# Optimization experiments

Hardware: AMD Instinct MI355X
Metric: run time of the kernel (lower is better)

The kernel has to match this reference:

```python
import jax, jax.numpy as jnp
import numpy as np

B, T, F, H, O = 256, 512, 128, 256, 1


def setup_inputs() -> dict:
    key = jax.random.key(0)
    ks = jax.random.split(key, 32)
    def rn(i, shape, s=0.05):
        return jax.random.normal(ks[i], shape, jnp.float32) * s
    inp = {
        "x": jax.random.normal(ks[0], (B, T, F), jnp.float32),
        # BatchNorm1d (eval mode) params / running stats
        "bn_gamma": 1.0 + rn(1, (F,), 0.1),
        "bn_beta": rn(2, (F,), 0.1),
        "bn_mean": rn(3, (F,), 0.1),
        "bn_var": 1.0 + jax.random.uniform(ks[4], (F,), jnp.float32) * 0.5,
        # SpatialAttention linear F->F
        "sa_W": rn(5, (F, F)), "sa_b": rn(6, (F,)),
        # layer_in F->H
        "in_W": rn(7, (H, F)), "in_b": rn(8, (H,)),
        # LSTM layer 0 (input H) and layer 1 (input H), torch gate order i,f,g,o
        "Wih0": rn(9, (4 * H, H)), "Whh0": rn(10, (4 * H, H)),
        "bih0": rn(11, (4 * H,)), "bhh0": rn(12, (4 * H,)),
        "Wih1": rn(13, (4 * H, H)), "Whh1": rn(14, (4 * H, H)),
        "bih1": rn(15, (4 * H,)), "bhh1": rn(16, (4 * H,)),
        # TemporalAttention: hidden_to_input H->F, T_A F->F
        "ta_hW": rn(17, (F, H)), "ta_hb": rn(18, (F,)),
        "ta_W": rn(19, (F, F)), "ta_b": rn(20, (F,)),
        # layer_out F->O, no bias
        "out_W": rn(21, (O, F)),
    }
    return inp


def _lstm_layer(seq, Wih, Whh, bih, bhh):
    # seq: [T, B, H_in]
    Hd = Whh.shape[1]
    b = bih + bhh
    def step(carry, xt):
        h, c = carry
        g = xt @ Wih.T + h @ Whh.T + b  # [B, 4H]
        i, f, gg, o = jnp.split(g, 4, axis=-1)
        c = jax.nn.sigmoid(f) * c + jax.nn.sigmoid(i) * jnp.tanh(gg)
        h = jax.nn.sigmoid(o) * jnp.tanh(c)
        return (h, c), h
    nb = seq.shape[1]
    init = (jnp.zeros((nb, Hd), seq.dtype), jnp.zeros((nb, Hd), seq.dtype))
    _, hs = jax.lax.scan(step, init, seq)
    return hs  # [T, B, H]


def reference(x, bn_gamma, bn_beta, bn_mean, bn_var, sa_W, sa_b, in_W, in_b,
              Wih0, Whh0, bih0, bhh0, Wih1, Whh1, bih1, bhh1,
              ta_hW, ta_hb, ta_W, ta_b, out_W):
    # BatchNorm1d (eval): normalize per feature
    xb = (x - bn_mean) * jax.lax.rsqrt(bn_var + 1e-5) * bn_gamma + bn_beta
    # Spatial attention (vectorized over all timesteps at once)
    alpha = jax.nn.softmax(jax.nn.sigmoid(xb @ sa_W.T + sa_b), axis=-1)
    xs = xb * alpha
    # layer_in (dropout is identity in eval mode)
    h = xs @ in_W.T + in_b  # [B, T, H]
    seq = jnp.swapaxes(h, 0, 1)  # [T, B, H]
    seq = _lstm_layer(seq, Wih0, Whh0, bih0, bhh0)
    seq = _lstm_layer(seq, Wih1, Whh1, bih1, bhh1)
    h_t = jnp.swapaxes(seq, 0, 1)  # [B, T, H]
    # Temporal attention
    total = h_t @ ta_hW.T + ta_hb  # [B, T, F]
    beta = jax.nn.softmax(jax.nn.relu(total @ ta_W.T + ta_b), axis=1)
    ctx = jnp.sum(beta * total, axis=1)  # [B, F]
    out = (ctx @ out_W.T).squeeze()  # [B]
    return out
```

## Files before the change

kernel.cpp:

```cpp
#include <hip/hip_runtime.h>

typedef __attribute__((ext_vector_type(8))) short short8;
typedef __attribute__((ext_vector_type(4))) float floatx4;
typedef __attribute__((ext_vector_type(2))) unsigned long long ull2;

__device__ __forceinline__ unsigned short f2bf(float f) {
  unsigned int u = __float_as_uint(f);
  unsigned int lsb = (u >> 16) & 1u;
  u += 0x7fffu + lsb;
  return (unsigned short)(u >> 16);
}
__device__ __forceinline__ float bf2f(unsigned short u) {
  unsigned int x = ((unsigned int)u) << 16;
  return __uint_as_float(x);
}
__device__ __forceinline__ float sigm(float x) { return 1.f / (1.f + __expf(-x)); }
__device__ __forceinline__ float tanh_fast(float x) { return 2.f / (1.f + __expf(-2.f * x)) - 1.f; }
__device__ __forceinline__ floatx4 mfma16(short8 a, short8 b, floatx4 c) {
  return __builtin_amdgcn_mfma_f32_16x16x32_bf16(a, b, c, 0, 0, 0);
}

__global__ __launch_bounds__(256) void prep_kernel(
    const float* __restrict__ Wih0, const float* __restrict__ inW,
    const float* __restrict__ inb, const float* __restrict__ bih0,
    const float* __restrict__ bhh0, const float* __restrict__ Whh0,
    const float* __restrict__ Whh1, const float* __restrict__ Wih1,
    const float* __restrict__ tahW, const float* __restrict__ taW,
    const float* __restrict__ bih1, const float* __restrict__ bhh1,
    unsigned short* __restrict__ Wc, float* __restrict__ bc,
    unsigned short* __restrict__ Whh0b, unsigned short* __restrict__ Whh1b,
    unsigned short* __restrict__ Wih1b, unsigned short* __restrict__ tahWb,
    unsigned short* __restrict__ taWb, float* __restrict__ b1) {
  const int b = blockIdx.x, tid = threadIdx.x;
  if (b < 512) {
    const int n = b * 2 + (tid >> 7), k = tid & 127;
    float a = 0.f;
    for (int j = 0; j < 256; ++j) a += Wih0[n * 256 + j] * inW[j * 128 + k];
    Wc[n * 128 + k] = f2bf(a);
    if (k == 0) {
      float bs = bih0[n] + bhh0[n];
      for (int j = 0; j < 256; ++j) bs += Wih0[n * 256 + j] * inb[j];
      bc[n] = bs;
    }
  } else if (b < 896) {
    const int bb = b - 512;
    const float* src = (bb < 128) ? Whh0 : (bb < 256) ? Whh1 : Wih1;
    unsigned short* dst = (bb < 128) ? Whh0b : (bb < 256) ? Whh1b : Wih1b;
    const int off = (bb & 127) * 2048 + tid * 8;
    short8 v;
#pragma unroll
    for (int u = 0; u < 8; ++u) v[u] = (short)f2bf(src[off + u]);
    *(short8*)&dst[off] = v;
  } else if (b < 912) {
    const int off = (b - 896) * 2048 + tid * 8;
    short8 v;
#pragma unroll
    for (int u = 0; u < 8; ++u) v[u] = (short)f2bf(tahW[off + u]);
    *(short8*)&tahWb[off] = v;
  } else if (b < 920) {
    const int off = (b - 912) * 2048 + tid * 8;
    short8 v;
#pragma unroll
    for (int u = 0; u < 8; ++u) v[u] = (short)f2bf(taW[off + u]);
    *(short8*)&taWb[off] = v;
  } else {
#pragma unroll
    for (int u = 0; u < 4; ++u) {
      const int i = tid * 4 + u;
      b1[i] = bih1[i] + bhh1[i];
    }
  }
}

__global__ __launch_bounds__(256) void bnsa_kernel(
    const float* __restrict__ x, const float* __restrict__ gamma,
    const float* __restrict__ beta, const float* __restrict__ mean,
    const float* __restrict__ var, const float* __restrict__ saW,
    const float* __restrict__ sab, unsigned short* __restrict__ xs) {
  __shared__ unsigned short saWs[128 * 132];
  __shared__ unsigned short xbb[128 * 136];
  const int tid = threadIdx.x;
  const int wv = tid >> 6, lane = tid & 63;
  const int lm = lane & 15, q = lane >> 4;
  const long r0 = (long)blockIdx.x * 128;

  for (int i = tid; i < 16384; i += 256) saWs[(i >> 7) * 132 + (i & 127)] = f2bf(saW[i]);
  {
    const int k0 = tid & 127;
    const float mn = mean[k0];
    const float is = rsqrtf(var[k0] + 1e-5f) * gamma[k0];
    const float bt = beta[k0];
    for (int i = tid; i < 16384; i += 256) {
      const int m = i >> 7;
      xbb[m * 136 + k0] = f2bf((x[(r0 + m) * 128 + k0] - mn) * is + bt);
    }
  }
  __syncthreads();

  short8 af[2][4];
#pragma unroll
  for (int mt = 0; mt < 2; ++mt)
#pragma unroll
    for (int kt = 0; kt < 4; ++kt)
      af[mt][kt] = *(const short8*)&xbb[(wv * 32 + mt * 16 + lm) * 136 + kt * 32 + q * 8];

  floatx4 acc[2][8];
#pragma unroll
  for (int nt = 0; nt < 8; ++nt) {
    const float sb = sab[nt * 16 + lm];
    short8 bf[4];
#pragma unroll
    for (int kt = 0; kt < 4; ++kt)
      bf[kt] = *(const short8*)&saWs[(nt * 16 + lm) * 132 + kt * 32 + q * 8];
#pragma unroll
    for (int mt = 0; mt < 2; ++mt) {
      floatx4 a = (floatx4){sb, sb, sb, sb};
#pragma unroll
      for (int kt = 0; kt < 4; ++kt) a = mfma16(af[mt][kt], bf[kt], a);
      acc[mt][nt] = a;
    }
  }
  float tot[2][4];
#pragma unroll
  for (int mt = 0; mt < 2; ++mt)
#pragma unroll
    for (int r = 0; r < 4; ++r) {
      float p = 0.f;
#pragma unroll
      for (int nt = 0; nt < 8; ++nt) {
        const float e = __expf(sigm(acc[mt][nt][r]));
        acc[mt][nt][r] = e;
        p += e;
      }
      p += __shfl_xor(p, 1);
      p += __shfl_xor(p, 2);
      p += __shfl_xor(p, 4);
      p += __shfl_xor(p, 8);
      tot[mt][r] = p;
    }
  __syncthreads();
  unsigned short* stg = saWs;
#pragma unroll
  for (int nt = 0; nt < 8; ++nt) {
    const int col = nt * 16 + lm;
    const float mn = mean[col];
    const float is = rsqrtf(var[col] + 1e-5f) * gamma[col];
    const float bt = beta[col];
#pragma unroll
    for (int mt = 0; mt < 2; ++mt)
#pragma unroll
      for (int r = 0; r < 4; ++r) {
        const int row = wv * 32 + mt * 16 + q * 4 + r;
        const float xb = (x[(r0 + row) * 128 + col] - mn) * is + bt;
        stg[row * 128 + col] = f2bf(xb * (acc[mt][nt][r] / tot[mt][r]));
      }
  }
  __syncthreads();
  for (int i = tid * 8; i < 16384; i += 2048)
    *(short8*)&xs[r0 * 128 + i] = *(const short8*)&stg[i];
}

__global__ __launch_bounds__(512, 2) void persist_kernel(
    const unsigned short* __restrict__ xs,
    const unsigned short* __restrict__ Wc, const float* __restrict__ bc,
    const unsigned short* __restrict__ Whh0,
    const unsigned short* __restrict__ Wih1, const float* __restrict__ b1,
    const unsigned short* __restrict__ Whh1,
    const unsigned short* __restrict__ tahWg, const float* __restrict__ tahb,
    const unsigned short* __restrict__ taWg, const float* __restrict__ tab,
    const float* __restrict__ outW,
    ull2* __restrict__ ex,
    float* __restrict__ out) {
  __shared__ unsigned short tahWs[128 * 264];
  __shared__ unsigned short taWs[128 * 136];
  __shared__ unsigned short h0buf[16 * 264];
  __shared__ unsigned short h1buf[16 * 264];
  __shared__ float gatebuf[2][8 * 16 * 20];
  __shared__ unsigned short totB[16 * 136];

  const int tid = threadIdx.x;
  const int wv = tid >> 6, lane = tid & 63;
  const int lm = lane & 15, q = lane >> 4;
  const int slice = blockIdx.x >> 4, group = blockIdx.x & 15;
  const int g = wv & 3, ht = wv >> 2;
  const int b0 = group * 16;
  const int hcol = slice * 32 + ht * 16 + lm;
  const int ng = g * 256 + hcol;
  const int fcol = wv * 16 + lm;

  for (int i = tid; i < 128 * 256; i += 512) tahWs[(i >> 8) * 264 + (i & 255)] = tahWg[i];
  for (int i = tid; i < 128 * 128; i += 512) taWs[(i >> 7) * 136 + (i & 127)] = taWg[i];
  for (int i = tid; i < 16 * 264; i += 512) { h0buf[i] = 0; h1buf[i] = 0; }

  short8 Wcf[4], W0f[8], W1if[8], W1hf[8];
#pragma unroll
  for (int kt = 0; kt < 4; ++kt) Wcf[kt] = *(const short8*)&Wc[(size_t)ng * 128 + kt * 32 + q * 8];
#pragma unroll
  for (int kt = 0; kt < 8; ++kt) {
    W0f[kt] = *(const short8*)&Whh0[(size_t)ng * 256 + kt * 32 + q * 8];
    W1if[kt] = *(const short8*)&Wih1[(size_t)ng * 256 + kt * 32 + q * 8];
    W1hf[kt] = *(const short8*)&Whh1[(size_t)ng * 256 + kt * 32 + q * 8];
  }
  const float bcv = bc[ng], b1v = b1[ng];
  const float tahbv = tahb[fcol], tabv = tab[fcol], outWv = outW[fcol];

  floatx4 cst0 = (floatx4){0.f, 0.f, 0.f, 0.f};
  floatx4 cst1 = (floatx4){0.f, 0.f, 0.f, 0.f};
  float num[4] = {0.f, 0.f, 0.f, 0.f}, den[4] = {0.f, 0.f, 0.f, 0.f};

  const unsigned short* xrow = xs + (size_t)(b0 + lm) * 65536 + q * 8;
  short8 axf[4], axn[4];
#pragma unroll
  for (int kt = 0; kt < 4; ++kt) axf[kt] = *(const short8*)(xrow + kt * 32);

  const int ew = ((slice >> 1) << 8) + (((slice & 1) * 32 + ht * 16 + lm) << 2) + q;
  ull2* const exg = ex + (size_t)group * 2048;

  const int npidx = ((wv >> 2) << 1) | (wv & 1);
  const int nt = npidx * 64 + lane;
  unsigned voBase[8];
#pragma unroll
  for (int L = 0; L < 2; ++L)
#pragma unroll
    for (int j = 0; j < 4; ++j) voBase[L * 4 + j] = (unsigned)((L * 1024 + j * 256 + nt) << 4);
  const int cb = nt >> 2, qq = nt & 3;

  __syncthreads();

  for (int t = 0; t <= 512; ++t) {
    const int p = t & 1;
    const unsigned fvu = (unsigned)(t + 1);

    {
      floatx4 aW = (floatx4){0.f, 0.f, 0.f, 0.f};
      floatx4 aH = (floatx4){bcv, bcv, bcv, bcv};
#pragma unroll
      for (int kt = 0; kt < 4; ++kt) aW = mfma16(axf[kt], Wcf[kt], aW);
#pragma unroll
      for (int kt = 0; kt < 8; ++kt) {
        const short8 a = *(const short8*)&h0buf[lm * 264 + kt * 32 + q * 8];
        aH = mfma16(a, W0f[kt], aH);
      }
      const floatx4 acc = aW + aH;
#pragma unroll
      for (int r = 0; r < 4; ++r) gatebuf[0][(wv * 16 + q * 4 + r) * 20 + lm] = acc[r];
    }
    {
      const size_t tn = (t < 511) ? t + 1 : 511;
#pragma unroll
      for (int kt = 0; kt < 4; ++kt) axn[kt] = *(const short8*)(xrow + tn * 128 + kt * 32);
    }
    {
      floatx4 aI = (floatx4){b1v, b1v, b1v, b1v};
      floatx4 aH = (floatx4){0.f, 0.f, 0.f, 0.f};
#pragma unroll
      for (int kt = 0; kt < 8; ++kt) {
        const short8 a = *(const short8*)&h0buf[lm * 264 + kt * 32 + q * 8];
        aI = mfma16(a, W1if[kt], aI);
      }
#pragma unroll
      for (int kt = 0; kt < 8; ++kt) {
        const short8 a = *(const short8*)&h1buf[lm * 264 + kt * 32 + q * 8];
        aH = mfma16(a, W1hf[kt], aH);
      }
      const floatx4 acc = aI + aH;
#pragma unroll
      for (int r = 0; r < 4; ++r) gatebuf[1][(wv * 16 + q * 4 + r) * 20 + lm] = acc[r];
    }
    __syncthreads();

    if (g < 2) {
      const int L = g;
      unsigned short hb[4];
      if (L == 0) {
#pragma unroll
        for (int r = 0; r < 4; ++r) {
          const int m = q * 4 + r;
          const float iv = gatebuf[0][((ht * 4 + 0) * 16 + m) * 20 + lm];
          const float fv = gatebuf[0][((ht * 4 + 1) * 16 + m) * 20 + lm];
          const float gv = gatebuf[0][((ht * 4 + 2) * 16 + m) * 20 + lm];
          const float ov = gatebuf[0][((ht * 4 + 3) * 16 + m) * 20 + lm];
          const float cn = sigm(fv) * cst0[r] + sigm(iv) * tanh_fast(gv);
          cst0[r] = cn;
          hb[r] = f2bf(sigm(ov) * tanh_fast(cn));
        }
      } else {
#pragma unroll
        for (int r = 0; r < 4; ++r) hb[r] = 0;
        if (t > 0) {
#pragma unroll
          for (int r = 0; r < 4; ++r) {
            const int m = q * 4 + r;
            const float iv = gatebuf[1][((ht * 4 + 0) * 16 + m) * 20 + lm];
            const float fv = gatebuf[1][((ht * 4 + 1) * 16 + m) * 20 + lm];
            const float gv = gatebuf[1][((ht * 4 + 2) * 16 + m) * 20 + lm];
            const float ov = gatebuf[1][((ht * 4 + 3) * 16 + m) * 20 + lm];
            const float cn = sigm(fv) * cst1[r] + sigm(iv) * tanh_fast(gv);
            cst1[r] = cn;
            hb[r] = f2bf(sigm(ov) * tanh_fast(cn));
          }
        }
      }
      const unsigned long long sq = (unsigned long long)fvu << 32;
      const unsigned long long qlo = (unsigned long long)hb[0] | ((unsigned long long)hb[1] << 16) | sq;
      const unsigned long long qhi = (unsigned long long)hb[2] | ((unsigned long long)hb[3] << 16) | sq;
      unsigned long long* wp =
          (unsigned long long*)(exg + (size_t)p * 32768 + (size_t)L * 1024 + ew);
      __hip_atomic_store(&wp[0], qlo, __ATOMIC_RELAXED, __HIP_MEMORY_SCOPE_AGENT);
      __hip_atomic_store(&wp[1], qhi, __ATOMIC_RELAXED, __HIP_MEMORY_SCOPE_AGENT);
    }

    floatx4 ta;
    if (t >= 2) {
      ta = (floatx4){tahbv, tahbv, tahbv, tahbv};
#pragma unroll
      for (int kt = 0; kt < 8; ++kt) {
        const short8 a = *(const short8*)&h1buf[lm * 264 + kt * 32 + q * 8];
        ta = mfma16(a, *(const short8*)&tahWs[fcol * 264 + kt * 32 + q * 8], ta);
      }
#pragma unroll
      for (int r = 0; r < 4; ++r) totB[(q * 4 + r) * 136 + fcol] = f2bf(ta[r]);
    }
    __syncthreads();
    if (t >= 2) {
      floatx4 sa = (floatx4){tabv, tabv, tabv, tabv};
#pragma unroll
      for (int kt = 0; kt < 4; ++kt) {
        const short8 a = *(const short8*)&totB[lm * 136 + kt * 32 + q * 8];
        sa = mfma16(a, *(const short8*)&taWs[fcol * 136 + kt * 32 + q * 8], sa);
      }
#pragma unroll
      for (int r = 0; r < 4; ++r) {
        const float e = __expf(fmaxf(sa[r], 0.f));
        num[r] += e * ta[r];
        den[r] += e;
      }
    }

    if (g >= 2) {
      const unsigned pterm = (unsigned)p << 19;
      const unsigned v0o = voBase[0] + pterm, v1o = voBase[1] + pterm;
      const unsigned v2o = voBase[2] + pterm, v3o = voBase[3] + pterm;
      const unsigned v4o = voBase[4] + pterm, v5o = voBase[5] + pterm;
      const unsigned v6o = voBase[6] + pterm, v7o = voBase[7] + pterm;
      ull2 d0, d1, d2, d3, e0, e1, e2, e3;
      unsigned bad;
      do {
        asm volatile(
            "global_load_dwordx4 %0, %8, %16 sc0 sc1\n\t"
            "global_load_dwordx4 %1, %9, %16 sc0 sc1\n\t"
            "global_load_dwordx4 %2, %10, %16 sc0 sc1\n\t"
            "global_load_dwordx4 %3, %11, %16 sc0 sc1\n\t"
            "global_load_dwordx4 %4, %12, %16 sc0 sc1\n\t"
            "global_load_dwordx4 %5, %13, %16 sc0 sc1\n\t"
            "global_load_dwordx4 %6, %14, %16 sc0 sc1\n\t"
            "global_load_dwordx4 %7, %15, %16 sc0 sc1\n\t"
            "s_waitcnt vmcnt(0)"
            : "=&v"(d0), "=&v"(d1), "=&v"(d2), "=&v"(d3),
              "=&v"(e0), "=&v"(e1), "=&v"(e2), "=&v"(e3)
            : "v"(v0o), "v"(v1o), "v"(v2o), "v"(v3o),
              "v"(v4o), "v"(v5o), "v"(v6o), "v"(v7o),
              "s"(exg)
            : "memory");
        bad = ((unsigned)(d0.x >> 32) != fvu) | ((unsigned)(d0.y >> 32) != fvu) |
              ((unsigned)(d1.x >> 32) != fvu) | ((unsigned)(d1.y >> 32) != fvu) |
              ((unsigned)(d2.x >> 32) != fvu) | ((unsigned)(d2.y >> 32) != fvu) |
              ((unsigned)(d3.x >> 32) != fvu) | ((unsigned)(d3.y >> 32) != fvu) |
              ((unsigned)(e0.x >> 32) != fvu) | ((unsigned)(e0.y >> 32) != fvu) |
              ((unsigned)(e1.x >> 32) != fvu) | ((unsigned)(e1.y >> 32) != fvu) |
              ((unsigned)(e2.x >> 32) != fvu) | ((unsigned)(e2.y >> 32) != fvu) |
              ((unsigned)(e3.x >> 32) != fvu) | ((unsigned)(e3.y >> 32) != fvu);
      } while (bad);
      {
        const int c0 = cb, c1 = 64 + cb, c2 = 128 + cb, c3 = 192 + cb;
        h0buf[(qq * 4 + 0) * 264 + c0] = (unsigned short)d0.x;
        h0buf[(qq * 4 + 1) * 264 + c0] = (unsigned short)(d0.x >> 16);
        h0buf[(qq * 4 + 2) * 264 + c0] = (unsigned short)d0.y;
        h0buf[(qq * 4 + 3) * 264 + c0] = (unsigned short)(d0.y >> 16);
        h0buf[(qq * 4 + 0) * 264 + c1] = (unsigned short)d1.x;
        h0buf[(qq * 4 + 1) * 264 + c1] = (unsigned short)(d1.x >> 16);
        h0buf[(qq * 4 + 2) * 264 + c1] = (unsigned short)d1.y;
        h0buf[(qq * 4 + 3) * 264 + c1] = (unsigned short)(d1.y >> 16);
        h0buf[(qq * 4 + 0) * 264 + c2] = (unsigned short)d2.x;
        h0buf[(qq * 4 + 1) * 264 + c2] = (unsigned short)(d2.x >> 16);
        h0buf[(qq * 4 + 2) * 264 + c2] = (unsigned short)d2.y;
        h0buf[(qq * 4 + 3) * 264 + c2] = (unsigned short)(d2.y >> 16);
        h0buf[(qq * 4 + 0) * 264 + c3] = (unsigned short)d3.x;
        h0buf[(qq * 4 + 1) * 264 + c3] = (unsigned short)(d3.x >> 16);
        h0buf[(qq * 4 + 2) * 264 + c3] = (unsigned short)d3.y;
        h0buf[(qq * 4 + 3) * 264 + c3] = (unsigned short)(d3.y >> 16);
        h1buf[(qq * 4 + 0) * 264 + c0] = (unsigned short)e0.x;
        h1buf[(qq * 4 + 1) * 264 + c0] = (unsigned short)(e0.x >> 16);
        h1buf[(qq * 4 + 2) * 264 + c0] = (unsigned short)e0.y;
        h1buf[(qq * 4 + 3) * 264 + c0] = (unsigned short)(e0.y >> 16);
        h1buf[(qq * 4 + 0) * 264 + c1] = (unsigned short)e1.x;
        h1buf[(qq * 4 + 1) * 264 + c1] = (unsigned short)(e1.x >> 16);
        h1buf[(qq * 4 + 2) * 264 + c1] = (unsigned short)e1.y;
        h1buf[(qq * 4 + 3) * 264 + c1] = (unsigned short)(e1.y >> 16);
        h1buf[(qq * 4 + 0) * 264 + c2] = (unsigned short)e2.x;
        h1buf[(qq * 4 + 1) * 264 + c2] = (unsigned short)(e2.x >> 16);
        h1buf[(qq * 4 + 2) * 264 + c2] = (unsigned short)e2.y;
        h1buf[(qq * 4 + 3) * 264 + c2] = (unsigned short)(e2.y >> 16);
        h1buf[(qq * 4 + 0) * 264 + c3] = (unsigned short)e3.x;
        h1buf[(qq * 4 + 1) * 264 + c3] = (unsigned short)(e3.x >> 16);
        h1buf[(qq * 4 + 2) * 264 + c3] = (unsigned short)e3.y;
        h1buf[(qq * 4 + 3) * 264 + c3] = (unsigned short)(e3.y >> 16);
      }
    }
    __syncthreads();

#pragma unroll
    for (int kt = 0; kt < 4; ++kt) axf[kt] = axn[kt];
  }

  {
    floatx4 ta = (floatx4){tahbv, tahbv, tahbv, tahbv};
#pragma unroll
    for (int kt = 0; kt < 8; ++kt) {
      const short8 a = *(const short8*)&h1buf[lm * 264 + kt * 32 + q * 8];
      ta = mfma16(a, *(const short8*)&tahWs[fcol * 264 + kt * 32 + q * 8], ta);
    }
#pragma unroll
    for (int r = 0; r < 4; ++r) totB[(q * 4 + r) * 136 + fcol] = f2bf(ta[r]);
    __syncthreads();
    floatx4 sa = (floatx4){tabv, tabv, tabv, tabv};
#pragma unroll
    for (int kt = 0; kt < 4; ++kt) {
      const short8 a = *(const short8*)&totB[lm * 136 + kt * 32 + q * 8];
      sa = mfma16(a, *(const short8*)&taWs[fcol * 136 + kt * 32 + q * 8], sa);
    }
#pragma unroll
    for (int r = 0; r < 4; ++r) {
      const float e = __expf(fmaxf(sa[r], 0.f));
      num[r] += e * ta[r];
      den[r] += e;
    }
  }
  __syncthreads();

  float* red = &gatebuf[0][0];
#pragma unroll
  for (int r = 0; r < 4; ++r) red[(q * 4 + r) * 136 + fcol] = (num[r] / den[r]) * outWv;
  __syncthreads();
  if (slice == 0 && tid < 16) {
    float s = 0.f;
    for (int k = 0; k < 128; ++k) s += red[tid * 136 + k];
    out[b0 + tid] = s;
  }
}

extern "C" void kernel_launch(void* const* d_in, const int* in_sizes, int n_in,
                              void* d_out, int out_size, void* d_ws, size_t ws_size,
                              hipStream_t stream) {
  (void)in_sizes; (void)n_in; (void)out_size; (void)ws_size;
  const float* x    = (const float*)d_in[0];
  const float* bng  = (const float*)d_in[1];
  const float* bnb  = (const float*)d_in[2];
  const float* bnm  = (const float*)d_in[3];
  const float* bnv  = (const float*)d_in[4];
  const float* saW  = (const float*)d_in[5];
  const float* sab  = (const float*)d_in[6];
  const float* inW  = (const float*)d_in[7];
  const float* inb  = (const float*)d_in[8];
  const float* Wih0 = (const float*)d_in[9];
  const float* Whh0 = (const float*)d_in[10];
  const float* bih0 = (const float*)d_in[11];
  const float* bhh0 = (const float*)d_in[12];
  const float* Wih1 = (const float*)d_in[13];
  const float* Whh1 = (const float*)d_in[14];
  const float* bih1 = (const float*)d_in[15];
  const float* bhh1 = (const float*)d_in[16];
  const float* tahW = (const float*)d_in[17];
  const float* tahb = (const float*)d_in[18];
  const float* taW  = (const float*)d_in[19];
  const float* tab  = (const float*)d_in[20];
  const float* outW = (const float*)d_in[21];
  float* out = (float*)d_out;

  char* ws = (char*)d_ws;
  size_t off = 0;
  auto alloc = [&](size_t bytes) {
    char* p = ws + off;
    off += (bytes + 255) & ~(size_t)255;
    return p;
  };
  unsigned short* Wc    = (unsigned short*)alloc((size_t)1024 * 128 * 2);
  float* bc             = (float*)alloc(1024 * 4);
  float* b1             = (float*)alloc(1024 * 4);
  unsigned short* Whh0b = (unsigned short*)alloc((size_t)1024 * 256 * 2);
  unsigned short* Whh1b = (unsigned short*)alloc((size_t)1024 * 256 * 2);
  unsigned short* Wih1b = (unsigned short*)alloc((size_t)1024 * 256 * 2);
  unsigned short* tahWb = (unsigned short*)alloc((size_t)128 * 256 * 2);
  unsigned short* taWb  = (unsigned short*)alloc((size_t)128 * 128 * 2);
  unsigned short* xs    = (unsigned short*)alloc((size_t)131072 * 128 * 2);
  ull2* ex              = (ull2*)alloc((size_t)2 * 16 * 2 * 1024 * 16);

  hipLaunchKernelGGL(prep_kernel, dim3(921), dim3(256), 0, stream, Wih0, inW, inb, bih0, bhh0,
                     Whh0, Whh1, Wih1, tahW, taW, bih1, bhh1, Wc, bc, Whh0b, Whh1b, Wih1b,
                     tahWb, taWb, b1);
  hipLaunchKernelGGL(bnsa_kernel, dim3(1024), dim3(256), 0, stream, x, bng, bnb, bnm, bnv, saW,
                     sab, xs);
  hipLaunchKernelGGL(persist_kernel, dim3(128), dim3(512), 0, stream, xs, Wc, bc, Whh0b, Wih1b,
                     b1, Whh1b, tahWb, tahb, taWb, tab, outW, ex, out);
}
```

Before: 2.001 ms.

## Double-buffer LSTM hidden state and overlap temporal attention with exchange polling

Splits the h0/h1 shared-memory buffers into ping-pong pairs so that reads of the current step and writes of the next step no longer collide. This removes one __syncthreads per timestep. The temporal-attention MFMA work moves onto the gate-computing waves (g<2), each covering two feature columns, while the other waves poll the cross-block exchange, so attention runs alongside the spin-wait. An s_sleep is added to the polling loop to reduce memory contention. The cost is more LDS use and more work on half the waves.

Result: slower. 2.709 ms (+35.3%).

```diff
diff --git a/kernel.cpp b/kernel.cpp
--- a/kernel.cpp
+++ b/kernel.cpp
@@ -173,9 +173,9 @@
     float* __restrict__ out) {
   __shared__ unsigned short tahWs[128 * 264];
   __shared__ unsigned short taWs[128 * 136];
-  __shared__ unsigned short h0buf[16 * 264];
-  __shared__ unsigned short h1buf[16 * 264];
-  __shared__ float gatebuf[2][8 * 16 * 20];
+  __shared__ unsigned short h0s[2][16 * 264];
+  __shared__ unsigned short h1s[2][16 * 264];
+  __shared__ float gatebuf[2][2560];
   __shared__ unsigned short totB[16 * 136];
 
   const int tid = threadIdx.x;
@@ -186,11 +186,12 @@
   const int b0 = group * 16;
   const int hcol = slice * 32 + ht * 16 + lm;
   const int ng = g * 256 + hcol;
-  const int fcol = wv * 16 + lm;
 
   for (int i = tid; i < 128 * 256; i += 512) tahWs[(i >> 8) * 264 + (i & 255)] = tahWg[i];
   for (int i = tid; i < 128 * 128; i += 512) taWs[(i >> 7) * 136 + (i & 127)] = taWg[i];
-  for (int i = tid; i < 16 * 264; i += 512) { h0buf[i] = 0; h1buf[i] = 0; }
+  for (int i = tid; i < 16 * 264; i += 512) {
+    h0s[0][i] = 0; h0s[1][i] = 0; h1s[0][i] = 0; h1s[1][i] = 0;
+  }
 
   short8 Wcf[4], W0f[8], W1if[8], W1hf[8];
 #pragma unroll
@@ -202,11 +203,20 @@
     W1hf[kt] = *(const short8*)&Whh1[(size_t)ng * 256 + kt * 32 + q * 8];
   }
   const float bcv = bc[ng], b1v = b1[ng];
-  const float tahbv = tahb[fcol], tabv = tab[fcol], outWv = outW[fcol];
+
+  const int widx = (wv & 1) | ((wv >> 2) << 1);
+  const int fc0 = (widx * 2) * 16 + lm, fc1 = (widx * 2 + 1) * 16 + lm;
+  float tahb0 = 0.f, tahb1 = 0.f, tab0 = 0.f, tab1 = 0.f, outW0 = 0.f, outW1 = 0.f;
+  if (g < 2) {
+    tahb0 = tahb[fc0]; tahb1 = tahb[fc1];
+    tab0 = tab[fc0];   tab1 = tab[fc1];
+    outW0 = outW[fc0]; outW1 = outW[fc1];
+  }
 
   floatx4 cst0 = (floatx4){0.f, 0.f, 0.f, 0.f};
   floatx4 cst1 = (floatx4){0.f, 0.f, 0.f, 0.f};
-  float num[4] = {0.f, 0.f, 0.f, 0.f}, den[4] = {0.f, 0.f, 0.f, 0.f};
+  float num0[4] = {0.f, 0.f, 0.f, 0.f}, den0[4] = {0.f, 0.f, 0.f, 0.f};
+  float num1[4] = {0.f, 0.f, 0.f, 0.f}, den1[4] = {0.f, 0.f, 0.f, 0.f};
 
   const unsigned short* xrow = xs + (size_t)(b0 + lm) * 65536 + q * 8;
   short8 axf[4], axn[4];
@@ -230,6 +240,10 @@
   for (int t = 0; t <= 512; ++t) {
     const int p = t & 1;
     const unsigned fvu = (unsigned)(t + 1);
+    const unsigned short* h0r = h0s[t & 1];
+    const unsigned short* h1r = h1s[t & 1];
+    unsigned short* h0w = h0s[(t + 1) & 1];
+    unsigned short* h1w = h1s[(t + 1) & 1];
 
     {
       floatx4 aW = (floatx4){0.f, 0.f, 0.f, 0.f};
@@ -238,7 +252,7 @@
       for (int kt = 0; kt < 4; ++kt) aW = mfma16(axf[kt], Wcf[kt], aW);
 #pragma unroll
       for (int kt = 0; kt < 8; ++kt) {
-        const short8 a = *(const short8*)&h0buf[lm * 264 + kt * 32 + q * 8];
+        const short8 a = *(const short8*)&h0r[lm * 264 + kt * 32 + q * 8];
         aH = mfma16(a, W0f[kt], aH);
       }
       const floatx4 acc = aW + aH;
@@ -255,12 +269,12 @@
       floatx4 aH = (floatx4){0.f, 0.f, 0.f, 0.f};
 #pragma unroll
       for (int kt = 0; kt < 8; ++kt) {
-        const short8 a = *(const short8*)&h0buf[lm * 264 + kt * 32 + q * 8];
+        const short8 a = *(const short8*)&h0r[lm * 264 + kt * 32 + q * 8];
         aI = mfma16(a, W1if[kt], aI);
       }
 #pragma unroll
       for (int kt = 0; kt < 8; ++kt) {
-        const short8 a = *(const short8*)&h1buf[lm * 264 + kt * 32 + q * 8];
+        const short8 a = *(const short8*)&h1r[lm * 264 + kt * 32 + q * 8];
         aH = mfma16(a, W1hf[kt], aH);
       }
       const floatx4 acc = aI + aH;
@@ -269,6 +283,7 @@
     }
     __syncthreads();
 
+    floatx4 ta0, ta1;
     if (g < 2) {
       const int L = g;
       unsigned short hb[4];
@@ -308,36 +323,23 @@
           (unsigned long long*)(exg + (size_t)p * 32768 + (size_t)L * 1024 + ew);
       __hip_atomic_store(&wp[0], qlo, __ATOMIC_RELAXED, __HIP_MEMORY_SCOPE_AGENT);
       __hip_atomic_store(&wp[1], qhi, __ATOMIC_RELAXED, __HIP_MEMORY_SCOPE_AGENT);
-    }
-
-    floatx4 ta;
-    if (t >= 2) {
-      ta = (floatx4){tahbv, tahbv, tahbv, tahbv};
-#pragma unroll
-      for (int kt = 0; kt < 8; ++kt) {
-        const short8 a = *(const short8*)&h1buf[lm * 264 + kt * 32 + q * 8];
-        ta = mfma16(a, *(const short8*)&tahWs[fcol * 264 + kt * 32 + q * 8], ta);
-      }
-#pragma unroll
-      for (int r = 0; r < 4; ++r) totB[(q * 4 + r) * 136 + fcol] = f2bf(ta[r]);
-    }
-    __syncthreads();
-    if (t >= 2) {
-      floatx4 sa = (floatx4){tabv, tabv, tabv, tabv};
-#pragma unroll
-      for (int kt = 0; kt < 4; ++kt) {
-        const short8 a = *(const short8*)&totB[lm * 136 + kt * 32 + q * 8];
-        sa = mfma16(a, *(const short8*)&taWs[fcol * 136 + kt * 32 + q * 8], sa);
-      }
-#pragma unroll
-      for (int r = 0; r < 4; ++r) {
-        const float e = __expf(fmaxf(sa[r], 0.f));
-        num[r] += e * ta[r];
-        den[r] += e;
-      }
-    }
-
-    if (g >= 2) {
+
+      if (t >= 2) {
+        ta0 = (floatx4){tahb0, tahb0, tahb0, tahb0};
+        ta1 = (floatx4){tahb1, tahb1, tahb1, tahb1};
+#pragma unroll
+        for (int kt = 0; kt < 8; ++kt) {
+          const short8 a = *(const short8*)&h1r[lm * 264 + kt * 32 + q * 8];
+          ta0 = mfma16(a, *(const short8*)&tahWs[fc0 * 264 + kt * 32 + q * 8], ta0);
+          ta1 = mfma16(a, *(const short8*)&tahWs[fc1 * 264 + kt * 32 + q * 8], ta1);
+        }
+#pragma unroll
+        for (int r = 0; r < 4; ++r) {
+          totB[(q * 4 + r) * 136 + fc0] = f2bf(ta0[r]);
+          totB[(q * 4 + r) * 136 + fc1] = f2bf(ta1[r]);
+        }
+      }
+    } else {
       const unsigned pterm = (unsigned)p << 19;
       const unsigned v0o = voBase[0] + pterm, v1o = voBase[1] + pterm;
       const unsigned v2o = voBase[2] + pterm, v3o = voBase[3] + pterm;
@@ -370,77 +372,119 @@
               ((unsigned)(e1.x >> 32) != fvu) | ((unsigned)(e1.y >> 32) != fvu) |
               ((unsigned)(e2.x >> 32) != fvu) | ((unsigned)(e2.y >> 32) != fvu) |
               ((unsigned)(e3.x >> 32) != fvu) | ((unsigned)(e3.y >> 32) != fvu);
+        if (bad) asm volatile("s_sleep 1");
       } while (bad);
       {
         const int c0 = cb, c1 = 64 + cb, c2 = 128 + cb, c3 = 192 + cb;
-        h0buf[(qq * 4 + 0) * 264 + c0] = (unsigned short)d0.x;
-        h0buf[(qq * 4 + 1) * 264 + c0] = (unsigned short)(d0.x >> 16);
-        h0buf[(qq * 4 + 2) * 264 + c0] = (unsigned short)d0.y;
-        h0buf[(qq * 4 + 3) * 264 + c0] = (unsigned short)(d0.y >> 16);
-        h0buf[(qq * 4 + 0) * 264 + c1] = (unsigned short)d1.x;
-        h0buf[(qq * 4 + 1) * 264 + c1] = (unsigned short)(d1.x >> 16);
-        h0buf[(qq * 4 + 2) * 264 + c1] = (unsigned short)d1.y;
-        h0buf[(qq * 4 + 3) * 264 + c1] = (unsigned short)(d1.y >> 16);
-        h0buf[(qq * 4 + 0) * 264 + c2] = (unsigned short)d2.x;
-        h0buf[(qq * 4 + 1) * 264 + c2] = (unsigned short)(d2.x >> 16);
-        h0buf[(qq * 4 + 2) * 264 + c2] = (unsigned short)d2.y;
-        h0buf[(qq * 4 + 3) * 264 + c2] = (unsigned short)(d2.y >> 16);
-        h0buf[(qq * 4 + 0) * 264 + c3] = (unsigned short)d3.x;
-        h0buf[(qq * 4 + 1) * 264 + c3] = (unsigned short)(d3.x >> 16);
-        h0buf[(qq * 4 + 2) * 264 + c3] = (unsigned short)d3.y;
-        h0buf[(qq * 4 + 3) * 264 + c3] = (unsigned short)(d3.y >> 16);
-        h1buf[(qq * 4 + 0) * 264 + c0] = (unsigned short)e0.x;
-        h1buf[(qq * 4 + 1) * 264 + c0] = (unsigned short)(e0.x >> 16);
-        h1buf[(qq * 4 + 2) * 264 + c0] = (unsigned short)e0.y;
-        h1buf[(qq * 4 + 3) * 264 + c0] = (unsigned short)(e0.y >> 16);
-        h1buf[(qq * 4 + 0) * 264 + c1] = (unsigned short)e1.x;
-        h1buf[(qq * 4 + 1) * 264 + c1] = (unsigned short)(e1.x >> 16);
-        h1buf[(qq * 4 + 2) * 264 + c1] = (unsigned short)e1.y;
-        h1buf[(qq * 4 + 3) * 264 + c1] = (unsigned short)(e1.y >> 16);
-        h1buf[(qq * 4 + 0) * 264 + c2] = (unsigned short)e2.x;
-        h1buf[(qq * 4 + 1) * 264 + c2] = (unsigned short)(e2.x >> 16);
-        h1buf[(qq * 4 + 2) * 264 + c2] = (unsigned short)e2.y;
-        h1buf[(qq * 4 + 3) * 264 + c2] = (unsigned short)(e2.y >> 16);
-        h1buf[(qq * 4 + 0) * 264 + c3] = (unsigned short)e3.x;
-        h1buf[(qq * 4 + 1) * 264 + c3] = (unsigned short)(e3.x >> 16);
-        h1buf[(qq * 4 + 2) * 264 + c3] = (unsigned short)e3.y;
-        h1buf[(qq * 4 + 3) * 264 + c3] = (unsigned short)(e3.y >> 16);
+        h0w[(qq * 4 + 0) * 264 + c0] = (unsigned short)d0.x;
+        h0w[(qq * 4 + 1) * 264 + c0] = (unsigned short)(d0.x >> 16);
+        h0w[(qq * 4 + 2) * 264 + c0] = (unsigned short)d0.y;
+        h0w[(qq * 4 + 3) * 264 + c0] = (unsigned short)(d0.y >> 16);
+        h0w[(qq * 4 + 0) * 264 + c1] = (unsigned short)d1.x;
+        h0w[(qq * 4 + 1) * 264 + c1] = (unsigned short)(d1.x >> 16);
+        h0w[(qq * 4 + 2) * 264 + c1] = (unsigned short)d1.y;
+        h0w[(qq * 4 + 3) * 264 + c1] = (unsigned short)(d1.y >> 16);
+        h0w[(qq * 4 + 0) * 264 + c2] = (unsigned short)d2.x;
+        h0w[(qq * 4 + 1) * 264 + c2] = (unsigned short)(d2.x >> 16);
+        h0w[(qq * 4 + 2) * 264 + c2] = (unsigned short)d2.y;
+        h0w[(qq * 4 + 3) * 264 + c2] = (unsigned short)(d2.y >> 16);
+        h0w[(qq * 4 + 0) * 264 + c3] = (unsigned short)d3.x;
+        h0w[(qq * 4 + 1) * 264 + c3] = (unsigned short)(d3.x >> 16);
+        h0w[(qq * 4 + 2) * 264 + c3] = (unsigned short)d3.y;
+        h0w[(qq * 4 + 3) * 264 + c3] = (unsigned short)(d3.y >> 16);
+        h1w[(qq * 4 + 0) * 264 + c0] = (unsigned short)e0.x;
+        h1w[(qq * 4 + 1) * 264 + c0] = (unsigned short)(e0.x >> 16);
+        h1w[(qq * 4 + 2) * 264 + c0] = (unsigned short)e0.y;
+        h1w[(qq * 4 + 3) * 264 + c0] = (unsigned short)(e0.y >> 16);
+        h1w[(qq * 4 + 0) * 264 + c1] = (unsigned short)e1.x;
+        h1w[(qq * 4 + 1) * 264 + c1] = (unsigned short)(e1.x >> 16);
+        h1w[(qq * 4 + 2) * 264 + c1] = (unsigned short)e1.y;
+        h1w[(qq * 4 + 3) * 264 + c1] = (unsigned short)(e1.y >> 16);
+        h1w[(qq * 4 + 0) * 264 + c2] = (unsigned short)e2.x;
+        h1w[(qq * 4 + 1) * 264 + c2] = (unsigned short)(e2.x >> 16);
+        h1w[(qq * 4 + 2) * 264 + c2] = (unsigned short)e2.y;
+        h1w[(qq * 4 + 3) * 264 + c2] = (unsigned short)(e2.y >> 16);
+        h1w[(qq * 4 + 0) * 264 + c3] = (unsigned short)e3.x;
+        h1w[(qq * 4 + 1) * 264 + c3] = (unsigned short)(e3.x >> 16);
+        h1w[(qq * 4 + 2) * 264 + c3] = (unsigned short)e3.y;
+        h1w[(qq * 4 + 3) * 264 + c3] = (unsigned short)(e3.y >> 16);
       }
     }
     __syncthreads();
 
+    if (g < 2 && t >= 2) {
+      floatx4 sa0 = (floatx4){tab0, tab0, tab0, tab0};
+      floatx4 sa1 = (floatx4){tab1, tab1, tab1, tab1};
+#pragma unroll
+      for (int kt = 0; kt < 4; ++kt) {
+        const short8 a = *(const short8*)&totB[lm * 136 + kt * 32 + q * 8];
+        sa0 = mfma16(a, *(const short8*)&taWs[fc0 * 136 + kt * 32 + q * 8], sa0);
+        sa1 = mfma16(a, *(const short8*)&taWs[fc1 * 136 + kt * 32 + q * 8], sa1);
+      }
+#pragma unroll
+      for (int r = 0; r < 4; ++r) {
+        const float e0v = __expf(fmaxf(sa0[r], 0.f));
+        num0[r] += e0v * ta0[r];
+        den0[r] += e0v;
+        const float e1v = __expf(fmaxf(sa1[r], 0.f));
+        num1[r] += e1v * ta1[r];
+        den1[r] += e1v;
+      }
+    }
+
 #pragma unroll
     for (int kt = 0; kt < 4; ++kt) axf[kt] = axn[kt];
   }
 
   {
-    floatx4 ta = (floatx4){tahbv, tahbv, tahbv, tahbv};
-#pragma unroll
-    for (int kt = 0; kt < 8; ++kt) {
-      const short8 a = *(const short8*)&h1buf[lm * 264 + kt * 32 + q * 8];
-      ta = mfma16(a, *(const short8*)&tahWs[fcol * 264 + kt * 32 + q * 8], ta);
-    }
-#pragma unroll
-    for (int r = 0; r < 4; ++r) totB[(q * 4 + r) * 136 + fcol] = f2bf(ta[r]);
+    floatx4 ta0t, ta1t;
+    if (g < 2) {
+      const unsigned short* h1r = h1s[1];
+      ta0t = (floatx4){tahb0, tahb0, tahb0, tahb0};
+      ta1t = (floatx4){tahb1, tahb1, tahb1, tahb1};
+#pragma unroll
+      for (int kt = 0; kt < 8; ++kt) {
+        const short8 a = *(const short8*)&h1r[lm * 264 + kt * 32 + q * 8];
+        ta0t = mfma16(a, *(const short8*)&tahWs[fc0 * 264 + kt * 32 + q * 8], ta0t);
+        ta1t = mfma16(a, *(const short8*)&tahWs[fc1 * 264 + kt * 32 + q * 8], ta1t);
+      }
+#pragma unroll
+      for (int r = 0; r < 4; ++r) {
+        totB[(q * 4 + r) * 136 + fc0] = f2bf(ta0t[r]);
+        totB[(q * 4 + r) * 136 + fc1] = f2bf(ta1t[r]);
+      }
+    }
     __syncthreads();
-    floatx4 sa = (floatx4){tabv, tabv, tabv, tabv};
-#pragma unroll
-    for (int kt = 0; kt < 4; ++kt) {
-      const short8 a = *(const short8*)&totB[lm * 136 + kt * 32 + q * 8];
-      sa = mfma16(a, *(const short8*)&taWs[fcol * 136 + kt * 32 + q * 8], sa);
-    }
+    if (g < 2) {
+      floatx4 sa0 = (floatx4){tab0, tab0, tab0, tab0};
+      floatx4 sa1 = (floatx4){tab1, tab1, tab1, tab1};
+#pragma unroll
+      for (int kt = 0; kt < 4; ++kt) {
+        const short8 a = *(const short8*)&totB[lm * 136 + kt * 32 + q * 8];
+        sa0 = mfma16(a, *(const short8*)&taWs[fc0 * 136 + kt * 32 + q * 8], sa0);
+        sa1 = mfma16(a, *(const short8*)&taWs[fc1 * 136 + kt * 32 + q * 8], sa1);
+      }
+#pragma unroll
+      for (int r = 0; r < 4; ++r) {
+        const float e0v = __expf(fmaxf(sa0[r], 0.f));
+        num0[r] += e0v * ta0t[r];
+        den0[r] += e0v;
+        const float e1v = __expf(fmaxf(sa1[r], 0.f));
+        num1[r] += e1v * ta1t[r];
+        den1[r] += e1v;
+      }
+    }
+  }
+  __syncthreads();
+
+  float* red = &gatebuf[0][0];
+  if (g < 2) {
 #pragma unroll
     for (int r = 0; r < 4; ++r) {
-      const float e = __expf(fmaxf(sa[r], 0.f));
-      num[r] += e * ta[r];
-      den[r] += e;
-    }
-  }
-  __syncthreads();
-
-  float* red = &gatebuf[0][0];
-#pragma unroll
-  for (int r = 0; r < 4; ++r) red[(q * 4 + r) * 136 + fcol] = (num[r] / den[r]) * outWv;
+      red[(q * 4 + r) * 136 + fc0] = (num0[r] / den0[r]) * outW0;
+      red[(q * 4 + r) * 136 + fc1] = (num1[r] / den1[r]) * outW1;
+    }
+  }
   __syncthreads();
   if (slice == 0 && tid < 16) {
     float s = 0.f;
```

## Halve persistent grid to 64 blocks of 1024 threads, each owning 64 hidden columns

Applied to the files above, without the earlier changes.

The persistent LSTM kernel now runs 64 workgroups of 1024 threads, so each block owns 64 hidden columns instead of 32. This halves the number of blocks exchanging hidden-state slices through global memory each timestep, and each wave polls fewer remote slices. It also narrows the gate buffer padding from 20 to 17 and restricts the temporal-attention work to the first 8 waves. In exchange each block carries heavier per-step barriers, and more per-thread register pressure may build under the 1024-thread launch bound.

After: 6.585 ms. 3.29x slower.

```diff
diff --git a/kernel.cpp b/kernel.cpp
--- a/kernel.cpp
+++ b/kernel.cpp
@@ -160,7 +160,7 @@
     *(short8*)&xs[r0 * 128 + i] = *(const short8*)&stg[i];
 }
 
-__global__ __launch_bounds__(512, 2) void persist_kernel(
+__global__ __launch_bounds__(1024) void persist_kernel(
     const unsigned short* __restrict__ xs,
     const unsigned short* __restrict__ Wc, const float* __restrict__ bc,
     const unsigned short* __restrict__ Whh0,
@@ -175,7 +175,7 @@
   __shared__ unsigned short taWs[128 * 136];
   __shared__ unsigned short h0buf[16 * 264];
   __shared__ unsigned short h1buf[16 * 264];
-  __shared__ float gatebuf[2][8 * 16 * 20];
+  __shared__ float gatebuf[2][4352];
   __shared__ unsigned short totB[16 * 136];
 
   const int tid = threadIdx.x;
@@ -184,13 +184,13 @@
   const int slice = blockIdx.x >> 4, group = blockIdx.x & 15;
   const int g = wv & 3, ht = wv >> 2;
   const int b0 = group * 16;
-  const int hcol = slice * 32 + ht * 16 + lm;
+  const int hcol = slice * 64 + ht * 16 + lm;
   const int ng = g * 256 + hcol;
-  const int fcol = wv * 16 + lm;
-
-  for (int i = tid; i < 128 * 256; i += 512) tahWs[(i >> 8) * 264 + (i & 255)] = tahWg[i];
-  for (int i = tid; i < 128 * 128; i += 512) taWs[(i >> 7) * 136 + (i & 127)] = taWg[i];
-  for (int i = tid; i < 16 * 264; i += 512) { h0buf[i] = 0; h1buf[i] = 0; }
+  const int fcol = (wv & 7) * 16 + lm;
+
+  for (int i = tid; i < 128 * 256; i += 1024) tahWs[(i >> 8) * 264 + (i & 255)] = tahWg[i];
+  for (int i = tid; i < 128 * 128; i += 1024) taWs[(i >> 7) * 136 + (i & 127)] = taWg[i];
+  for (int i = tid; i < 16 * 264; i += 1024) { h0buf[i] = 0; h1buf[i] = 0; }
 
   short8 Wcf[4], W0f[8], W1if[8], W1hf[8];
 #pragma unroll
@@ -213,17 +213,18 @@
 #pragma unroll
   for (int kt = 0; kt < 4; ++kt) axf[kt] = *(const short8*)(xrow + kt * 32);
 
-  const int ew = ((slice >> 1) << 8) + (((slice & 1) * 32 + ht * 16 + lm) << 2) + q;
+  const int ew = slice * 256 + (ht * 16 + lm) * 4 + q;
   ull2* const exg = ex + (size_t)group * 2048;
 
   const int npidx = ((wv >> 2) << 1) | (wv & 1);
   const int nt = npidx * 64 + lane;
-  unsigned voBase[8];
+  unsigned voBase[4];
 #pragma unroll
   for (int L = 0; L < 2; ++L)
 #pragma unroll
-    for (int j = 0; j < 4; ++j) voBase[L * 4 + j] = (unsigned)((L * 1024 + j * 256 + nt) << 4);
-  const int cb = nt >> 2, qq = nt & 3;
+    for (int j = 0; j < 2; ++j) voBase[L * 2 + j] = (unsigned)((L * 1024 + j * 512 + nt) << 4);
+  const int cb = (nt >> 8) * 64 + ((nt >> 2) & 63);
+  const int qq = nt & 3;
 
   __syncthreads();
 
@@ -243,7 +244,7 @@
       }
       const floatx4 acc = aW + aH;
 #pragma unroll
-      for (int r = 0; r < 4; ++r) gatebuf[0][(wv * 16 + q * 4 + r) * 20 + lm] = acc[r];
+      for (int r = 0; r < 4; ++r) gatebuf[0][(wv * 16 + q * 4 + r) * 17 + lm] = acc[r];
     }
     {
       const size_t tn = (t < 511) ? t + 1 : 511;
@@ -265,7 +266,7 @@
       }
       const floatx4 acc = aI + aH;
 #pragma unroll
-      for (int r = 0; r < 4; ++r) gatebuf[1][(wv * 16 + q * 4 + r) * 20 + lm] = acc[r];
+      for (int r = 0; r < 4; ++r) gatebuf[1][(wv * 16 + q * 4 + r) * 17 + lm] = acc[r];
     }
     __syncthreads();
 
@@ -276,10 +277,10 @@
 #pragma unroll
         for (int r = 0; r < 4; ++r) {
           const int m = q * 4 + r;
-          const float iv = gatebuf[0][((ht * 4 + 0) * 16 + m) * 20 + lm];
-          const float fv = gatebuf[0][((ht * 4 + 1) * 16 + m) * 20 + lm];
-          const float gv = gatebuf[0][((ht * 4 + 2) * 16 + m) * 20 + lm];
-          const float ov = gatebuf[0][((ht * 4 + 3) * 16 + m) * 20 + lm];
+          const float iv = gatebuf[0][((ht * 4 + 0) * 16 + m) * 17 + lm];
+          const float fv = gatebuf[0][((ht * 4 + 1) * 16 + m) * 17 + lm];
+          const float gv = gatebuf[0][((ht * 4 + 2) * 16 + m) * 17 + lm];
+          const float ov = gatebuf[0][((ht * 4 + 3) * 16 + m) * 17 + lm];
           const float cn = sigm(fv) * cst0[r] + sigm(iv) * tanh_fast(gv);
           cst0[r] = cn;
           hb[r] = f2bf(sigm(ov) * tanh_fast(cn));
@@ -291,10 +292,10 @@
 #pragma unroll
           for (int r = 0; r < 4; ++r) {
             const int m = q * 4 + r;
-            const float iv = gatebuf[1][((ht * 4 + 0) * 16 + m) * 20 + lm];
-            const float fv = gatebuf[1][((ht * 4 + 1) * 16 + m) * 20 + lm];
-            const float gv = gatebuf[1][((ht * 4 + 2) * 16 + m) * 20 + lm];
-            const float ov = gatebuf[1][((ht * 4 + 3) * 16 + m) * 20 + lm];
+            const float iv = gatebuf[1][((ht * 4 + 0) * 16 + m) * 17 + lm];
+            const float fv = gatebuf[1][((ht * 4 + 1) * 16 + m) * 17 + lm];
+            const float gv = gatebuf[1][((ht * 4 + 2) * 16 + m) * 17 + lm];
+            const float ov = gatebuf[1][((ht * 4 + 3) * 16 + m) * 17 + lm];
             const float cn = sigm(fv) * cst1[r] + sigm(iv) * tanh_fast(gv);
             cst1[r] = cn;
             hb[r] = f2bf(sigm(ov) * tanh_fast(cn));
@@ -311,7 +312,7 @@
     }
 
     floatx4 ta;
-    if (t >= 2) {
+    if (wv < 8 && t >= 2) {
       ta = (floatx4){tahbv, tahbv, tahbv, tahbv};
 #pragma unroll
       for (int kt = 0; kt < 8; ++kt) {
@@ -322,7 +323,7 @@
       for (int r = 0; r < 4; ++r) totB[(q * 4 + r) * 136 + fcol] = f2bf(ta[r]);
     }
     __syncthreads();
-    if (t >= 2) {
+    if (wv < 8 && t >= 2) {
       floatx4 sa = (floatx4){tabv, tabv, tabv, tabv};
 #pragma unroll
       for (int kt = 0; kt < 4; ++kt) {
@@ -341,38 +342,26 @@
       const unsigned pterm = (unsigned)p << 19;
       const unsigned v0o = voBase[0] + pterm, v1o = voBase[1] + pterm;
       const unsigned v2o = voBase[2] + pterm, v3o = voBase[3] + pterm;
-      const unsigned v4o = voBase[4] + pterm, v5o = voBase[5] + pterm;
-      const unsigned v6o = voBase[6] + pterm, v7o = voBase[7] + pterm;
-      ull2 d0, d1, d2, d3, e0, e1, e2, e3;
+      ull2 d0, d1, e0, e1;
       unsigned bad;
       do {
         asm volatile(
-            "global_load_dwordx4 %0, %8, %16 sc0 sc1\n\t"
-            "global_load_dwordx4 %1, %9, %16 sc0 sc1\n\t"
-            "global_load_dwordx4 %2, %10, %16 sc0 sc1\n\t"
-            "global_load_dwordx4 %3, %11, %16 sc0 sc1\n\t"
-            "global_load_dwordx4 %4, %12, %16 sc0 sc1\n\t"
-            "global_load_dwordx4 %5, %13, %16 sc0 sc1\n\t"
-            "global_load_dwordx4 %6, %14, %16 sc0 sc1\n\t"
-            "global_load_dwordx4 %7, %15, %16 sc0 sc1\n\t"
+            "global_load_dwordx4 %0, %4, %8 sc0 sc1\n\t"
+            "global_load_dwordx4 %1, %5, %8 sc0 sc1\n\t"
+            "global_load_dwordx4 %2, %6, %8 sc0 sc1\n\t"
+            "global_load_dwordx4 %3, %7, %8 sc0 sc1\n\t"
             "s_waitcnt vmcnt(0)"
-            : "=&v"(d0), "=&v"(d1), "=&v"(d2), "=&v"(d3),
-              "=&v"(e0), "=&v"(e1), "=&v"(e2), "=&v"(e3)
+            : "=&v"(d0), "=&v"(d1), "=&v"(e0), "=&v"(e1)
             : "v"(v0o), "v"(v1o), "v"(v2o), "v"(v3o),
-              "v"(v4o), "v"(v5o), "v"(v6o), "v"(v7o),
               "s"(exg)
             : "memory");
         bad = ((unsigned)(d0.x >> 32) != fvu) | ((unsigned)(d0.y >> 32) != fvu) |
               ((unsigned)(d1.x >> 32) != fvu) | ((unsigned)(d1.y >> 32) != fvu) |
-              ((unsigned)(d2.x >> 32) != fvu) | ((unsigned)(d2.y >> 32) != fvu) |
-              ((unsigned)(d3.x >> 32) != fvu) | ((unsigned)(d3.y >> 32) != fvu) |
               ((unsigned)(e0.x >> 32) != fvu) | ((unsigned)(e0.y >> 32) != fvu) |
-              ((unsigned)(e1.x >> 32) != fvu) | ((unsigned)(e1.y >> 32) != fvu) |
-              ((unsigned)(e2.x >> 32) != fvu) | ((unsigned)(e2.y >> 32) != fvu) |
-              ((unsigned)(e3.x >> 32) != fvu) | ((unsigned)(e3.y >> 32) != fvu);
+              ((unsigned)(e1.x >> 32) != fvu) | ((unsigned)(e1.y >> 32) != fvu);
       } while (bad);
       {
-        const int c0 = cb, c1 = 64 + cb, c2 = 128 + cb, c3 = 192 + cb;
+        const int c0 = cb, c1 = cb + 128;
         h0buf[(qq * 4 + 0) * 264 + c0] = (unsigned short)d0.x;
         h0buf[(qq * 4 + 1) * 264 + c0] = (unsigned short)(d0.x >> 16);
         h0buf[(qq * 4 + 2) * 264 + c0] = (unsigned short)d0.y;
@@ -381,14 +370,6 @@
         h0buf[(qq * 4 + 1) * 264 + c1] = (unsigned short)(d1.x >> 16);
         h0buf[(qq * 4 + 2) * 264 + c1] = (unsigned short)d1.y;
         h0buf[(qq * 4 + 3) * 264 + c1] = (unsigned short)(d1.y >> 16);
-        h0buf[(qq * 4 + 0) * 264 + c2] = (unsigned short)d2.x;
-        h0buf[(qq * 4 + 1) * 264 + c2] = (unsigned short)(d2.x >> 16);
-        h0buf[(qq * 4 + 2) * 264 + c2] = (unsigned short)d2.y;
-        h0buf[(qq * 4 + 3) * 264 + c2] = (unsigned short)(d2.y >> 16);
-        h0buf[(qq * 4 + 0) * 264 + c3] = (unsigned short)d3.x;
-        h0buf[(qq * 4 + 1) * 264 + c3] = (unsigned short)(d3.x >> 16);
-        h0buf[(qq * 4 + 2) * 264 + c3] = (unsigned short)d3.y;
-        h0buf[(qq * 4 + 3) * 264 + c3] = (unsigned short)(d3.y >> 16);
         h1buf[(qq * 4 + 0) * 264 + c0] = (unsigned short)e0.x;
         h1buf[(qq * 4 + 1) * 264 + c0] = (unsigned short)(e0.x >> 16);
         h1buf[(qq * 4 + 2) * 264 + c0] = (unsigned short)e0.y;
@@ -397,14 +378,6 @@
         h1buf[(qq * 4 + 1) * 264 + c1] = (unsigned short)(e1.x >> 16);
         h1buf[(qq * 4 + 2) * 264 + c1] = (unsigned short)e1.y;
         h1buf[(qq * 4 + 3) * 264 + c1] = (unsigned short)(e1.y >> 16);
-        h1buf[(qq * 4 + 0) * 264 + c2] = (unsigned short)e2.x;
-        h1buf[(qq * 4 + 1) * 264 + c2] = (unsigned short)(e2.x >> 16);
-        h1buf[(qq * 4 + 2) * 264 + c2] = (unsigned short)e2.y;
-        h1buf[(qq * 4 + 3) * 264 + c2] = (unsigned short)(e2.y >> 16);
-        h1buf[(qq * 4 + 0) * 264 + c3] = (unsigned short)e3.x;
-        h1buf[(qq * 4 + 1) * 264 + c3] = (unsigned short)(e3.x >> 16);
-        h1buf[(qq * 4 + 2) * 264 + c3] = (unsigned short)e3.y;
-        h1buf[(qq * 4 + 3) * 264 + c3] = (unsigned short)(e3.y >> 16);
       }
     }
     __syncthreads();
@@ -413,7 +386,7 @@
     for (int kt = 0; kt < 4; ++kt) axf[kt] = axn[kt];
   }
 
-  {
+  if (wv < 8) {
     floatx4 ta = (floatx4){tahbv, tahbv, tahbv, tahbv};
 #pragma unroll
     for (int kt = 0; kt < 8; ++kt) {
@@ -435,12 +408,16 @@
       num[r] += e * ta[r];
       den[r] += e;
     }
+  } else {
+    __syncthreads();
   }
   __syncthreads();
 
   float* red = &gatebuf[0][0];
-#pragma unroll
-  for (int r = 0; r < 4; ++r) red[(q * 4 + r) * 136 + fcol] = (num[r] / den[r]) * outWv;
+  if (wv < 8) {
+#pragma unroll
+    for (int r = 0; r < 4; ++r) red[(q * 4 + r) * 136 + fcol] = (num[r] / den[r]) * outWv;
+  }
   __syncthreads();
   if (slice == 0 && tid < 16) {
     float s = 0.f;
@@ -500,6 +477,6 @@
                      tahWb, taWb, b1);
   hipLaunchKernelGGL(bnsa_kernel, dim3(1024), dim3(256), 0, stream, x, bng, bnb, bnm, bnv, saW,
                      sab, xs);
-  hipLaunchKernelGGL(persist_kernel, dim3(128), dim3(512), 0, stream, xs, Wc, bc, Whh0b, Wih1b,
+  hipLaunchKernelGGL(persist_kernel, dim3(64), dim3(1024), 0, stream, xs, Wc, bc, Whh0b, Wih1b,
                      b1, Whh1b, tahWb, tahb, taWb, tab, outW, ex, out);
 }
```
